# Kernel optimization log

Measured on AMD Instinct MI355X. Metric: run time of the kernel, lower is better.

The kernel has to match this reference:

```python
import jax, jax.numpy as jnp
import numpy as np
from jax import lax

B = 128      # batch
T = 80       # video frames
FEAT = 4096  # VGG feature dim
E_H = 512    # encoder hidden
D_H = 512    # decoder hidden
OHL = 3000   # vocab / one-hot length


def lstm(xs, h0, c0, Wih, Whh, b):
    """Single-layer LSTM over leading time axis. xs: (S, B, In). PyTorch gate order i,f,g,o."""
    def step(carry, x):
        h, c = carry
        gates = x @ Wih.T + h @ Whh.T + b  # (B, 4H)
        i, f, g, o = jnp.split(gates, 4, axis=-1)
        c = jax.nn.sigmoid(f) * c + jax.nn.sigmoid(i) * jnp.tanh(g)
        h = jax.nn.sigmoid(o) * jnp.tanh(c)
        return (h, c), h
    (h, c), ys = lax.scan(step, (h0, c0), xs)
    return ys, h, c


def setup_inputs() -> dict:
    key = jax.random.key(0)
    ks = jax.random.split(key, 16)
    def w(k, shape, fan):
        return (jax.random.normal(k, shape, jnp.float32) / np.sqrt(fan)).astype(jnp.float32)
    return {
        "input_feature": jax.random.normal(ks[0], (B, T, FEAT), jnp.float32),
        "correct_answer": jax.random.normal(ks[1], (44, B, OHL), jnp.float32),
        "We_ih": w(ks[2], (4 * E_H, FEAT), E_H),
        "We_hh": w(ks[3], (4 * E_H, E_H), E_H),
        "be_ih": w(ks[4], (4 * E_H,), E_H),
        "be_hh": w(ks[5], (4 * E_H,), E_H),
        "Wd_ih": w(ks[6], (4 * D_H, E_H + D_H), D_H),
        "Wd_hh": w(ks[7], (4 * D_H, D_H), D_H),
        "bd_ih": w(ks[8], (4 * D_H,), D_H),
        "bd_hh": w(ks[9], (4 * D_H,), D_H),
        "Wi": w(ks[10], (D_H, OHL), OHL),
        "bi": w(ks[11], (D_H,), OHL),
        "Wo": w(ks[12], (OHL, D_H), D_H),
        "bo": w(ks[13], (OHL,), D_H),
        "max_len": 44,
    }


def reference(input_feature, correct_answer, We_ih, We_hh, be_ih, be_hh,
              Wd_ih, Wd_hh, bd_ih, bd_hh, Wi, bi, Wo, bo, max_len):
    be = be_ih + be_hh
    bd = bd_ih + bd_hh
    # torch .view(shape[1], shape[0], 4096) on contiguous tensor == reshape
    x = input_feature.reshape(T, B, FEAT)
    # Encoding phase
    h0e = jnp.zeros((B, E_H), x.dtype)
    enc_seq, he, ce = lstm(x, h0e, h0e, We_ih, We_hh, be)
    dec_in = jnp.concatenate([enc_seq, jnp.zeros((T, B, D_H), x.dtype)], axis=2)
    h0d = jnp.zeros((B, D_H), x.dtype)
    _, hd, cd = lstm(dec_in, h0d, h0d, Wd_ih, Wd_hh, bd)
    # Encoder over zero padding for the caption phase
    pad = jnp.zeros((max_len, B, FEAT), x.dtype)
    enc_pad, _, _ = lstm(pad, he, ce, We_ih, We_hh, be)
    # Decoder inputs: <BOS> one-hot at step 0, teacher-forced answers after (schedule=False)
    bos = jnp.zeros((1, B, OHL), x.dtype).at[:, :, -2].set(1.0)
    emb_bos = bos @ Wi.T + bi                               # (1, B, D_H)
    emb_ans = correct_answer[1:max_len] @ Wi.T + bi         # (max_len-1, B, D_H)
    samples = jnp.concatenate([emb_bos, emb_ans], axis=0)   # (max_len, B, D_H)
    dec_in2 = jnp.concatenate([samples, enc_pad], axis=2)   # (max_len, B, D_H+E_H)
    dec_out, _, _ = lstm(dec_in2, hd, cd, Wd_ih, Wd_hh, bd)
    words = dec_out @ Wo.T + bo                              # (max_len, B, OHL)
    return words
```

## Files before the change

### kernel.cpp

```cpp
#include <hip/hip_runtime.h>
#include <cmath>


typedef __bf16 bf16x8 __attribute__((ext_vector_type(8)));
typedef float  f32x4  __attribute__((ext_vector_type(4)));

#define LDSROW 40

template<bool BIAS, bool ACCUM>
__global__ __launch_bounds__(256)
void gemm_split(const float* __restrict__ A, int lda,
                const float* __restrict__ Bw, int ldb,
                float* __restrict__ C, int ldc,
                const float* __restrict__ bias,
                int M, int N, int K)
{
    (void)M;
    __shared__ __bf16 sAh[128 * LDSROW], sAl[128 * LDSROW];
    __shared__ __bf16 sBh[128 * LDSROW], sBl[128 * LDSROW];

    const int tid  = threadIdx.x;
    const int lane = tid & 63;
    const int wid  = tid >> 6;
    const int m0 = blockIdx.x * 128, n0 = blockIdx.y * 128;
    const int wm = (wid >> 1) * 64, wn = (wid & 1) * 64;
    const int lr = lane & 15, lg = lane >> 4;

    const int srow = tid >> 1;
    const int scol = (tid & 1) * 16;

    f32x4 acc[4][4];
#pragma unroll
    for (int mt = 0; mt < 4; ++mt)
#pragma unroll
        for (int nt = 0; nt < 4; ++nt) acc[mt][nt] = (f32x4)(0.0f);

    const int KT = (K + 31) >> 5;
    for (int kt = 0; kt < KT; ++kt) {
        const int k0 = kt * 32;
        {
            const float* aptr = A + (size_t)(m0 + srow) * lda + k0 + scol;
            float x[16];
            if (k0 + scol + 16 <= K) {
                const f32x4* p = (const f32x4*)aptr;
                f32x4 v0 = p[0], v1 = p[1], v2 = p[2], v3 = p[3];
#pragma unroll
                for (int j = 0; j < 4; ++j) { x[j] = v0[j]; x[4+j] = v1[j]; x[8+j] = v2[j]; x[12+j] = v3[j]; }
            } else {
#pragma unroll
                for (int j = 0; j < 16; ++j) {
                    const int kk = k0 + scol + j;
                    x[j] = (kk < K) ? aptr[j] : 0.f;
                }
            }
#pragma unroll
            for (int j = 0; j < 16; ++j) {
                const float v = x[j];
                const __bf16 h = (__bf16)v;
                sAh[srow * LDSROW + scol + j] = h;
                sAl[srow * LDSROW + scol + j] = (__bf16)(v - (float)h);
            }
        }
        {
            const int nrow = n0 + srow;
            const float* bptr = Bw + (size_t)nrow * ldb + k0 + scol;
            float x[16];
            if (nrow < N && k0 + scol + 16 <= K) {
                const f32x4* p = (const f32x4*)bptr;
                f32x4 v0 = p[0], v1 = p[1], v2 = p[2], v3 = p[3];
#pragma unroll
                for (int j = 0; j < 4; ++j) { x[j] = v0[j]; x[4+j] = v1[j]; x[8+j] = v2[j]; x[12+j] = v3[j]; }
            } else {
#pragma unroll
                for (int j = 0; j < 16; ++j) {
                    const int kk = k0 + scol + j;
                    x[j] = (nrow < N && kk < K) ? bptr[j] : 0.f;
                }
            }
#pragma unroll
            for (int j = 0; j < 16; ++j) {
                const float v = x[j];
                const __bf16 h = (__bf16)v;
                sBh[srow * LDSROW + scol + j] = h;
                sBl[srow * LDSROW + scol + j] = (__bf16)(v - (float)h);
            }
        }
        __syncthreads();

        bf16x8 ah[4], al[4], bh[4], bl[4];
#pragma unroll
        for (int t = 0; t < 4; ++t) {
            ah[t] = *(const bf16x8*)&sAh[(wm + t * 16 + lr) * LDSROW + lg * 8];
            al[t] = *(const bf16x8*)&sAl[(wm + t * 16 + lr) * LDSROW + lg * 8];
            bh[t] = *(const bf16x8*)&sBh[(wn + t * 16 + lr) * LDSROW + lg * 8];
            bl[t] = *(const bf16x8*)&sBl[(wn + t * 16 + lr) * LDSROW + lg * 8];
        }
#pragma unroll
        for (int mt = 0; mt < 4; ++mt)
#pragma unroll
            for (int nt = 0; nt < 4; ++nt) {
                f32x4 a_ = acc[mt][nt];
                a_ = __builtin_amdgcn_mfma_f32_16x16x32_bf16(ah[mt], bh[nt], a_, 0, 0, 0);
                a_ = __builtin_amdgcn_mfma_f32_16x16x32_bf16(ah[mt], bl[nt], a_, 0, 0, 0);
                a_ = __builtin_amdgcn_mfma_f32_16x16x32_bf16(al[mt], bh[nt], a_, 0, 0, 0);
                acc[mt][nt] = a_;
            }
        __syncthreads();
    }

#pragma unroll
    for (int mt = 0; mt < 4; ++mt)
#pragma unroll
        for (int nt = 0; nt < 4; ++nt)
#pragma unroll
            for (int r = 0; r < 4; ++r) {
                const int m = m0 + wm + mt * 16 + lg * 4 + r;
                const int n = n0 + wn + nt * 16 + lr;
                if (n < N) {
                    float v = acc[mt][nt][r];
                    if (BIAS) v += bias[n];
                    if (ACCUM) v += C[(size_t)m * ldc + n];
                    C[(size_t)m * ldc + n] = v;
                }
            }
}

__global__ __launch_bounds__(256)
void lstm_step(const float* __restrict__ gpre,
               const float* __restrict__ bias,
               const float* __restrict__ Whh,
               const float* __restrict__ h_prev,
               float* __restrict__ c,
               float* __restrict__ h_out)
{
    __shared__ float h_s[16][36];
    __shared__ float w_s[64][36];
    const int tid = threadIdx.x;
    const int jj = tid & 15, bb = tid >> 4;
    const int j = blockIdx.x * 16 + jj;
    const int b = blockIdx.y * 16 + bb;

    float a0 = 0.f, a1 = 0.f, a2 = 0.f, a3 = 0.f;

    const int hr = tid >> 4, hc = (tid & 15) * 2;
    const int wr = tid >> 2, wc = (tid & 3) * 8;
    const int wg = wr >> 4, wj = wr & 15;
    const float* hsrc = h_prev + (size_t)(blockIdx.y * 16 + hr) * 512 + hc;
    const float* wsrc = Whh + (size_t)(wg * 512 + blockIdx.x * 16 + wj) * 512 + wc;

    for (int kt = 0; kt < 16; ++kt) {
        const int k0 = kt * 32;
        {
            const float2 hv = *(const float2*)(hsrc + k0);
            h_s[hr][hc] = hv.x; h_s[hr][hc + 1] = hv.y;
            const f32x4 w0 = *(const f32x4*)(wsrc + k0);
            const f32x4 w1 = *(const f32x4*)(wsrc + k0 + 4);
#pragma unroll
            for (int q = 0; q < 4; ++q) { w_s[wr][wc + q] = w0[q]; w_s[wr][wc + 4 + q] = w1[q]; }
        }
        __syncthreads();
#pragma unroll
        for (int k = 0; k < 32; ++k) {
            const float hvk = h_s[bb][k];
            a0 += hvk * w_s[ 0 + jj][k];
            a1 += hvk * w_s[16 + jj][k];
            a2 += hvk * w_s[32 + jj][k];
            a3 += hvk * w_s[48 + jj][k];
        }
        __syncthreads();
    }

    float pi = 0.f, pf = 0.f, pg = 0.f, po = 0.f;
    if (gpre) {
        const float* g = gpre + (size_t)b * 2048 + j;
        pi = g[0]; pf = g[512]; pg = g[1024]; po = g[1536];
    }
    if (bias) { pi += bias[j]; pf += bias[j + 512]; pg += bias[j + 1024]; po += bias[j + 1536]; }
    pi += a0; pf += a1; pg += a2; po += a3;

    const float ig = 1.f / (1.f + __expf(-pi));
    const float fg = 1.f / (1.f + __expf(-pf));
    const float gg = tanhf(pg);
    const float og = 1.f / (1.f + __expf(-po));

    const size_t ci = (size_t)b * 512 + j;
    const float cn = fg * c[ci] + ig * gg;
    c[ci] = cn;
    h_out[ci] = og * tanhf(cn);
}

__global__ void add2(const float* __restrict__ a, const float* __restrict__ b,
                     float* __restrict__ o, int n)
{
    const int i = blockIdx.x * 256 + threadIdx.x;
    if (i < n) o[i] = a[i] + b[i];
}

__global__ void emb_bos(const float* __restrict__ Wi, const float* __restrict__ bi,
                        float* __restrict__ emb)
{
    const int i = blockIdx.x * 256 + threadIdx.x;
    const int d = i & 511;
    emb[i] = Wi[(size_t)d * 3000 + 2998] + bi[d];
}

extern "C" void kernel_launch(void* const* d_in, const int* in_sizes, int n_in,
                              void* d_out, int out_size, void* d_ws, size_t ws_size,
                              hipStream_t stream)
{
    (void)in_sizes; (void)n_in; (void)out_size; (void)ws_size;
    const float* in_feat = (const float*)d_in[0];
    const float* ca      = (const float*)d_in[1];
    const float* We_ih   = (const float*)d_in[2];
    const float* We_hh   = (const float*)d_in[3];
    const float* be_ih   = (const float*)d_in[4];
    const float* be_hh   = (const float*)d_in[5];
    const float* Wd_ih   = (const float*)d_in[6];
    const float* Wd_hh   = (const float*)d_in[7];
    const float* bd_ih   = (const float*)d_in[8];
    const float* bd_hh   = (const float*)d_in[9];
    const float* Wi      = (const float*)d_in[10];
    const float* bi      = (const float*)d_in[11];
    const float* Wo      = (const float*)d_in[12];
    const float* bo      = (const float*)d_in[13];
    float* out = (float*)d_out;
    float* ws  = (float*)d_ws;

    float* be    = ws;
    float* bd    = be + 2048;
    float* Xbuf  = bd + 2048;
    float* encH  = Xbuf + (size_t)10240 * 2048;
    float* padH  = encH + (size_t)81 * 65536;
    float* doutH = padH + (size_t)45 * 65536;
    float* emb   = doutH + (size_t)45 * 65536;
    float* cE    = emb + (size_t)5632 * 512;
    float* cD    = cE + 65536;
    float* hd0   = cD + 65536;
    float* hd1   = hd0 + 65536;

    add2<<<dim3(8), dim3(256), 0, stream>>>(be_ih, be_hh, be, 2048);
    add2<<<dim3(8), dim3(256), 0, stream>>>(bd_ih, bd_hh, bd, 2048);

    hipMemsetAsync(encH, 0, 65536 * sizeof(float), stream);
    hipMemsetAsync(cE,   0, 65536 * sizeof(float), stream);
    hipMemsetAsync(cD,   0, 65536 * sizeof(float), stream);
    hipMemsetAsync(hd0,  0, 65536 * sizeof(float), stream);

    emb_bos<<<dim3(256), dim3(256), 0, stream>>>(Wi, bi, emb);

    gemm_split<true, false><<<dim3(80, 16), dim3(256), 0, stream>>>(
        in_feat, 4096, We_ih, 4096, Xbuf, 2048, be, 10240, 2048, 4096);

    gemm_split<true, false><<<dim3(43, 4), dim3(256), 0, stream>>>(
        ca + (size_t)128 * 3000, 3000, Wi, 3000, emb + (size_t)128 * 512, 512, bi,
        5504, 512, 3000);

    for (int t = 0; t < 80; ++t)
        lstm_step<<<dim3(32, 8), dim3(256), 0, stream>>>(
            Xbuf + (size_t)t * 262144, nullptr, We_hh,
            encH + (size_t)t * 65536, cE, encH + (size_t)(t + 1) * 65536);

    gemm_split<true, false><<<dim3(80, 16), dim3(256), 0, stream>>>(
        encH + 65536, 512, Wd_ih, 1024, Xbuf, 2048, bd, 10240, 2048, 512);

    for (int t = 0; t < 80; ++t) {
        float* hin  = (t & 1) ? hd1 : hd0;
        float* hout = (t & 1) ? hd0 : hd1;
        lstm_step<<<dim3(32, 8), dim3(256), 0, stream>>>(
            Xbuf + (size_t)t * 262144, nullptr, Wd_hh, hin, cD, hout);
    }

    for (int t = 0; t < 44; ++t) {
        const float* hin = (t == 0) ? (encH + (size_t)80 * 65536) : (padH + (size_t)t * 65536);
        lstm_step<<<dim3(32, 8), dim3(256), 0, stream>>>(
            nullptr, be, We_hh, hin, cE, padH + (size_t)(t + 1) * 65536);
    }

    gemm_split<true, false><<<dim3(44, 16), dim3(256), 0, stream>>>(
        emb, 512, Wd_ih, 1024, Xbuf, 2048, bd, 5632, 2048, 512);
    gemm_split<false, true><<<dim3(44, 16), dim3(256), 0, stream>>>(
        padH + 65536, 512, Wd_ih + 512, 1024, Xbuf, 2048, nullptr, 5632, 2048, 512);

    for (int t = 0; t < 44; ++t) {
        const float* hin = (t == 0) ? hd0 : (doutH + (size_t)t * 65536);
        lstm_step<<<dim3(32, 8), dim3(256), 0, stream>>>(
            Xbuf + (size_t)t * 262144, nullptr, Wd_hh, hin, cD, doutH + (size_t)(t + 1) * 65536);
    }

    gemm_split<true, false><<<dim3(44, 24), dim3(256), 0, stream>>>(
        doutH + 65536, 512, Wo, 512, out, 3000, bo, 5632, 3000, 512);
}
```

Before: 6.988 ms.

## Fuse all LSTM recurrences into one persistent kernel with grid barriers

Replaces the 248 per-timestep lstm_step launches with a single persistent 128-block kernel. The encoder and decoder run as a wavefront on separate halves of the grid, and steps are separated by an atomic grid barrier. Each block keeps its slice of the recurrent weights in LDS as bf16 and runs MFMA with a hi/lo split of h to keep close to fp32 accuracy. This removes launch overhead and the repeated weight reloads, but it relies on all 128 blocks being co-resident, and the weights are rounded to bf16.

```diff
diff --git a/kernel.cpp b/kernel.cpp
--- a/kernel.cpp
+++ b/kernel.cpp
@@ -6,6 +6,8 @@
 typedef float  f32x4  __attribute__((ext_vector_type(4)));
 
 #define LDSROW 40
+#define SLOT   65536
+#define NBLK   128
 
 template<bool BIAS, bool ACCUM>
 __global__ __launch_bounds__(256)
@@ -125,68 +127,207 @@
             }
 }
 
-__global__ __launch_bounds__(256)
-void lstm_step(const float* __restrict__ gpre,
-               const float* __restrict__ bias,
-               const float* __restrict__ Whh,
-               const float* __restrict__ h_prev,
-               float* __restrict__ c,
-               float* __restrict__ h_out)
-{
-    __shared__ float h_s[16][36];
-    __shared__ float w_s[64][36];
+
+__device__ __forceinline__ void gbar(unsigned* cnt, unsigned* gen)
+{
+    __syncthreads();
+    if (threadIdx.x == 0) {
+        __threadfence();
+        const unsigned g = __hip_atomic_load(gen, __ATOMIC_RELAXED, __HIP_MEMORY_SCOPE_AGENT);
+        const unsigned a = __hip_atomic_fetch_add(cnt, 1u, __ATOMIC_ACQ_REL, __HIP_MEMORY_SCOPE_AGENT);
+        if (a == NBLK - 1) {
+            __hip_atomic_store(cnt, 0u, __ATOMIC_RELAXED, __HIP_MEMORY_SCOPE_AGENT);
+            __hip_atomic_store(gen, g + 1u, __ATOMIC_RELEASE, __HIP_MEMORY_SCOPE_AGENT);
+        } else {
+            while (__hip_atomic_load(gen, __ATOMIC_ACQUIRE, __HIP_MEMORY_SCOPE_AGENT) == g)
+                __builtin_amdgcn_s_sleep(1);
+        }
+        __threadfence();
+    }
+    __syncthreads();
+}
+
+template<int KT>
+__device__ __forceinline__ void gemm_phase(
+    const __bf16* __restrict__ sW, float* __restrict__ pg, int K,
+    const __bf16* __restrict__ s1h, const __bf16* __restrict__ s1l,
+    const __bf16* __restrict__ s2h, const __bf16* __restrict__ s2l)
+{
+    const int lane = threadIdx.x & 63, w = threadIdx.x >> 6;
+    const int lr = lane & 15, lg = lane >> 4;
+    const int kf = lg * 8;
+    const int mb = w * 32 + lr;
+
+    f32x4 acc[2][2];
+#pragma unroll
+    for (int mt = 0; mt < 2; ++mt)
+#pragma unroll
+        for (int nt = 0; nt < 2; ++nt) acc[mt][nt] = (f32x4)(0.0f);
+
+#pragma unroll 2
+    for (int kt = 0; kt < KT; ++kt) {
+        const int kk = kt * 32 + kf;
+        const __bf16* ph; const __bf16* pl; int ko;
+        if (kk < 512) { ph = s1h; pl = s1l; ko = kk; }
+        else          { ph = s2h; pl = s2l; ko = kk - 512; }
+
+        const int n0 = lr, n1 = 16 + lr;
+        const bf16x8 b0 = *(const bf16x8*)&sW[(n0 * K + kt * 32 + kf) ^ ((n0 & 7) << 3)];
+        const bf16x8 b1 = *(const bf16x8*)&sW[(n1 * K + kt * 32 + kf) ^ ((n1 & 7) << 3)];
+#pragma unroll
+        for (int mt = 0; mt < 2; ++mt) {
+            const int m = mb + mt * 16;
+            const bf16x8 ah = *(const bf16x8*)&ph[m * 512 + ko];
+            const bf16x8 al = *(const bf16x8*)&pl[m * 512 + ko];
+            acc[mt][0] = __builtin_amdgcn_mfma_f32_16x16x32_bf16(ah, b0, acc[mt][0], 0, 0, 0);
+            acc[mt][0] = __builtin_amdgcn_mfma_f32_16x16x32_bf16(al, b0, acc[mt][0], 0, 0, 0);
+            acc[mt][1] = __builtin_amdgcn_mfma_f32_16x16x32_bf16(ah, b1, acc[mt][1], 0, 0, 0);
+            acc[mt][1] = __builtin_amdgcn_mfma_f32_16x16x32_bf16(al, b1, acc[mt][1], 0, 0, 0);
+        }
+    }
+
+#pragma unroll
+    for (int mt = 0; mt < 2; ++mt)
+#pragma unroll
+        for (int nt = 0; nt < 2; ++nt)
+#pragma unroll
+            for (int r = 0; r < 4; ++r)
+                pg[(w * 32 + mt * 16 + lg * 4 + r) * 33 + nt * 16 + lr] = acc[mt][nt][r];
+}
+
+__device__ __forceinline__ void pointwise(
+    const float* __restrict__ pg, const float* __restrict__ gpre,
+    const float* __restrict__ bsl, float* __restrict__ c, int d0,
+    __bf16* __restrict__ hhi, __bf16* __restrict__ hlo, float* __restrict__ hf32)
+{
     const int tid = threadIdx.x;
-    const int jj = tid & 15, bb = tid >> 4;
-    const int j = blockIdx.x * 16 + jj;
-    const int b = blockIdx.y * 16 + bb;
-
-    float a0 = 0.f, a1 = 0.f, a2 = 0.f, a3 = 0.f;
-
-    const int hr = tid >> 4, hc = (tid & 15) * 2;
-    const int wr = tid >> 2, wc = (tid & 3) * 8;
-    const int wg = wr >> 4, wj = wr & 15;
-    const float* hsrc = h_prev + (size_t)(blockIdx.y * 16 + hr) * 512 + hc;
-    const float* wsrc = Whh + (size_t)(wg * 512 + blockIdx.x * 16 + wj) * 512 + wc;
-
-    for (int kt = 0; kt < 16; ++kt) {
-        const int k0 = kt * 32;
-        {
-            const float2 hv = *(const float2*)(hsrc + k0);
-            h_s[hr][hc] = hv.x; h_s[hr][hc + 1] = hv.y;
-            const f32x4 w0 = *(const f32x4*)(wsrc + k0);
-            const f32x4 w1 = *(const f32x4*)(wsrc + k0 + 4);
-#pragma unroll
-            for (int q = 0; q < 4; ++q) { w_s[wr][wc + q] = w0[q]; w_s[wr][wc + 4 + q] = w1[q]; }
-        }
-        __syncthreads();
-#pragma unroll
-        for (int k = 0; k < 32; ++k) {
-            const float hvk = h_s[bb][k];
-            a0 += hvk * w_s[ 0 + jj][k];
-            a1 += hvk * w_s[16 + jj][k];
-            a2 += hvk * w_s[32 + jj][k];
-            a3 += hvk * w_s[48 + jj][k];
-        }
-        __syncthreads();
-    }
-
-    float pi = 0.f, pf = 0.f, pg = 0.f, po = 0.f;
+    const int b = tid >> 1, hf = tid & 1;
+    float add_[4][4];
     if (gpre) {
-        const float* g = gpre + (size_t)b * 2048 + j;
-        pi = g[0]; pf = g[512]; pg = g[1024]; po = g[1536];
-    }
-    if (bias) { pi += bias[j]; pf += bias[j + 512]; pg += bias[j + 1024]; po += bias[j + 1536]; }
-    pi += a0; pf += a1; pg += a2; po += a3;
-
-    const float ig = 1.f / (1.f + __expf(-pi));
-    const float fg = 1.f / (1.f + __expf(-pf));
-    const float gg = tanhf(pg);
-    const float og = 1.f / (1.f + __expf(-po));
-
-    const size_t ci = (size_t)b * 512 + j;
-    const float cn = fg * c[ci] + ig * gg;
-    c[ci] = cn;
-    h_out[ci] = og * tanhf(cn);
+#pragma unroll
+        for (int g = 0; g < 4; ++g) {
+            const f32x4 v = *(const f32x4*)&gpre[b * 2048 + g * 512 + d0 + hf * 4];
+#pragma unroll
+            for (int j = 0; j < 4; ++j) add_[g][j] = v[j];
+        }
+    } else {
+#pragma unroll
+        for (int g = 0; g < 4; ++g)
+#pragma unroll
+            for (int j = 0; j < 4; ++j) add_[g][j] = bsl[g * 8 + hf * 4 + j];
+    }
+#pragma unroll
+    for (int j = 0; j < 4; ++j) {
+        const int dd = hf * 4 + j;
+        const float pi = pg[b * 33 +  0 + dd] + add_[0][j];
+        const float pf = pg[b * 33 +  8 + dd] + add_[1][j];
+        const float pG = pg[b * 33 + 16 + dd] + add_[2][j];
+        const float po = pg[b * 33 + 24 + dd] + add_[3][j];
+        const float ig = 1.f / (1.f + __expf(-pi));
+        const float fg = 1.f / (1.f + __expf(-pf));
+        const float gg = tanhf(pG);
+        const float og = 1.f / (1.f + __expf(-po));
+        c[j] = fg * c[j] + ig * gg;
+        const float h = og * tanhf(c[j]);
+        const int off = b * 512 + d0 + dd;
+        const __bf16 hh = (__bf16)h;
+        hhi[off] = hh;
+        hlo[off] = (__bf16)(h - (float)hh);
+        if (hf32) hf32[off] = h;
+    }
+}
+
+__global__ __launch_bounds__(256, 1)
+void recurrence_kernel(const float* __restrict__ gpreE, const float* __restrict__ gpre2,
+                       const float* __restrict__ We_hh, const float* __restrict__ Wd_ih,
+                       const float* __restrict__ Wd_hh,
+                       const float* __restrict__ be, const float* __restrict__ bd,
+                       __bf16* encHi, __bf16* encLo, __bf16* padHi, __bf16* padLo,
+                       __bf16* dHi, __bf16* dLo, float* doutW,
+                       unsigned* bar_cnt, unsigned* bar_gen)
+{
+    __shared__ __bf16 sW[32 * 1024];
+    __shared__ float  pg[128 * 33];
+    __shared__ float  bsl[32];
+
+    const int  bid    = blockIdx.x;
+    const bool is_dec = bid >= 64;
+    const int  d0     = (is_dec ? bid - 64 : bid) * 8;
+    const int  tid    = threadIdx.x;
+    const int  K      = is_dec ? 1024 : 512;
+
+    for (int idx = tid; idx < 32 * K; idx += 256) {
+        const int nn = idx / K;
+        const int kk = idx - nn * K;
+        const int gr = (nn >> 3) * 512 + d0 + (nn & 7);
+        float wv;
+        if (!is_dec) wv = We_hh[(size_t)gr * 512 + kk];
+        else         wv = (kk < 512) ? Wd_ih[(size_t)gr * 1024 + kk]
+                                     : Wd_hh[(size_t)gr * 512 + kk - 512];
+        sW[(nn * K + kk) ^ ((nn & 7) << 3)] = (__bf16)wv;
+    }
+    if (tid < 32) bsl[tid] = (is_dec ? bd : be)[(tid >> 3) * 512 + d0 + (tid & 7)];
+    __syncthreads();
+
+    float c[4] = {0.f, 0.f, 0.f, 0.f};
+
+    for (int p = 0; p <= 80; ++p) {
+        if (!is_dec) {
+            if (p < 80) {
+                gemm_phase<16>(sW, pg, 512,
+                               encHi + (p & 1) * SLOT, encLo + (p & 1) * SLOT,
+                               nullptr, nullptr);
+                __syncthreads();
+                pointwise(pg, gpreE + (size_t)p * 262144, bsl, c, d0,
+                          encHi + ((p + 1) & 1) * SLOT, encLo + ((p + 1) & 1) * SLOT, nullptr);
+            }
+        } else {
+            if (p >= 1) {
+                const int t = p - 1;
+                gemm_phase<32>(sW, pg, 1024,
+                               encHi + (p & 1) * SLOT, encLo + (p & 1) * SLOT,
+                               dHi + (t & 1) * SLOT, dLo + (t & 1) * SLOT);
+                __syncthreads();
+                pointwise(pg, nullptr, bsl, c, d0,
+                          dHi + ((t + 1) & 1) * SLOT, dLo + ((t + 1) & 1) * SLOT, nullptr);
+            }
+        }
+        gbar(bar_cnt, bar_gen);
+    }
+
+    if (is_dec) {
+        for (int idx = tid; idx < 32 * 512; idx += 256) {
+            const int nn = idx >> 9, kk = idx & 511;
+            const int gr = (nn >> 3) * 512 + d0 + (nn & 7);
+            sW[(nn * 1024 + kk) ^ ((nn & 7) << 3)] = (__bf16)Wd_ih[(size_t)gr * 1024 + 512 + kk];
+        }
+    }
+    __syncthreads();
+
+    for (int q = 0; q <= 44; ++q) {
+        if (!is_dec) {
+            if (q < 44) {
+                const __bf16* sh = (q == 0) ? encHi : padHi + (q & 1) * SLOT;
+                const __bf16* sl = (q == 0) ? encLo : padLo + (q & 1) * SLOT;
+                gemm_phase<16>(sW, pg, 512, sh, sl, nullptr, nullptr);
+                __syncthreads();
+                pointwise(pg, nullptr, bsl, c, d0,
+                          padHi + ((q + 1) & 1) * SLOT, padLo + ((q + 1) & 1) * SLOT, nullptr);
+            }
+        } else {
+            if (q >= 1) {
+                const int u = q - 1;
+                gemm_phase<32>(sW, pg, 1024,
+                               padHi + (q & 1) * SLOT, padLo + (q & 1) * SLOT,
+                               dHi + (u & 1) * SLOT, dLo + (u & 1) * SLOT);
+                __syncthreads();
+                pointwise(pg, gpre2 + (size_t)u * 262144, bsl, c, d0,
+                          dHi + ((u + 1) & 1) * SLOT, dLo + ((u + 1) & 1) * SLOT,
+                          doutW + (size_t)u * SLOT);
+            }
+        }
+        gbar(bar_cnt, bar_gen);
+    }
 }
 
 __global__ void add2(const float* __restrict__ a, const float* __restrict__ b,
@@ -228,65 +369,44 @@
 
     float* be    = ws;
     float* bd    = be + 2048;
-    float* Xbuf  = bd + 2048;
-    float* encH  = Xbuf + (size_t)10240 * 2048;
-    float* padH  = encH + (size_t)81 * 65536;
-    float* doutH = padH + (size_t)45 * 65536;
-    float* emb   = doutH + (size_t)45 * 65536;
-    float* cE    = emb + (size_t)5632 * 512;
-    float* cD    = cE + 65536;
-    float* hd0   = cD + 65536;
-    float* hd1   = hd0 + 65536;
+    float* gpreE = bd + 2048;
+    float* gpre2 = gpreE + (size_t)80 * 262144;
+    float* emb   = gpre2 + (size_t)44 * 262144;
+    float* doutW = emb + (size_t)5632 * 512;
+    float* bf16z = doutW + (size_t)5632 * 512;
+    __bf16* encHi = (__bf16*)bf16z;
+    __bf16* encLo = encHi + 2 * SLOT;
+    __bf16* padHi = encLo + 2 * SLOT;
+    __bf16* padLo = padHi + 2 * SLOT;
+    __bf16* dHi   = padLo + 2 * SLOT;
+    __bf16* dLo   = dHi + 2 * SLOT;
+    unsigned* bar = (unsigned*)(dLo + 2 * SLOT);
 
     add2<<<dim3(8), dim3(256), 0, stream>>>(be_ih, be_hh, be, 2048);
     add2<<<dim3(8), dim3(256), 0, stream>>>(bd_ih, bd_hh, bd, 2048);
 
-    hipMemsetAsync(encH, 0, 65536 * sizeof(float), stream);
-    hipMemsetAsync(cE,   0, 65536 * sizeof(float), stream);
-    hipMemsetAsync(cD,   0, 65536 * sizeof(float), stream);
-    hipMemsetAsync(hd0,  0, 65536 * sizeof(float), stream);
+    hipMemsetAsync(encHi, 0, SLOT * 2, stream);
+    hipMemsetAsync(encLo, 0, SLOT * 2, stream);
+    hipMemsetAsync(dHi,   0, SLOT * 2, stream);
+    hipMemsetAsync(dLo,   0, SLOT * 2, stream);
+    hipMemsetAsync(bar,   0, 8, stream);
 
     emb_bos<<<dim3(256), dim3(256), 0, stream>>>(Wi, bi, emb);
 
     gemm_split<true, false><<<dim3(80, 16), dim3(256), 0, stream>>>(
-        in_feat, 4096, We_ih, 4096, Xbuf, 2048, be, 10240, 2048, 4096);
+        in_feat, 4096, We_ih, 4096, gpreE, 2048, be, 10240, 2048, 4096);
 
     gemm_split<true, false><<<dim3(43, 4), dim3(256), 0, stream>>>(
         ca + (size_t)128 * 3000, 3000, Wi, 3000, emb + (size_t)128 * 512, 512, bi,
         5504, 512, 3000);
 
-    for (int t = 0; t < 80; ++t)
-        lstm_step<<<dim3(32, 8), dim3(256), 0, stream>>>(
-            Xbuf + (size_t)t * 262144, nullptr, We_hh,
-            encH + (size_t)t * 65536, cE, encH + (size_t)(t + 1) * 65536);
-
-    gemm_split<true, false><<<dim3(80, 16), dim3(256), 0, stream>>>(
-        encH + 65536, 512, Wd_ih, 1024, Xbuf, 2048, bd, 10240, 2048, 512);
-
-    for (int t = 0; t < 80; ++t) {
-        float* hin  = (t & 1) ? hd1 : hd0;
-        float* hout = (t & 1) ? hd0 : hd1;
-        lstm_step<<<dim3(32, 8), dim3(256), 0, stream>>>(
-            Xbuf + (size_t)t * 262144, nullptr, Wd_hh, hin, cD, hout);
-    }
-
-    for (int t = 0; t < 44; ++t) {
-        const float* hin = (t == 0) ? (encH + (size_t)80 * 65536) : (padH + (size_t)t * 65536);
-        lstm_step<<<dim3(32, 8), dim3(256), 0, stream>>>(
-            nullptr, be, We_hh, hin, cE, padH + (size_t)(t + 1) * 65536);
-    }
-
     gemm_split<true, false><<<dim3(44, 16), dim3(256), 0, stream>>>(
-        emb, 512, Wd_ih, 1024, Xbuf, 2048, bd, 5632, 2048, 512);
-    gemm_split<false, true><<<dim3(44, 16), dim3(256), 0, stream>>>(
-        padH + 65536, 512, Wd_ih + 512, 1024, Xbuf, 2048, nullptr, 5632, 2048, 512);
-
-    for (int t = 0; t < 44; ++t) {
-        const float* hin = (t == 0) ? hd0 : (doutH + (size_t)t * 65536);
-        lstm_step<<<dim3(32, 8), dim3(256), 0, stream>>>(
-            Xbuf + (size_t)t * 262144, nullptr, Wd_hh, hin, cD, doutH + (size_t)(t + 1) * 65536);
-    }
+        emb, 512, Wd_ih, 1024, gpre2, 2048, bd, 5632, 2048, 512);
+
+    recurrence_kernel<<<dim3(NBLK), dim3(256), 0, stream>>>(
+        gpreE, gpre2, We_hh, Wd_ih, Wd_hh, be, bd,
+        encHi, encLo, padHi, padLo, dHi, dLo, doutW, bar, bar + 1);
 
     gemm_split<true, false><<<dim3(44, 24), dim3(256), 0, stream>>>(
-        doutH + 65536, 512, Wo, 512, out, 3000, bo, 5632, 3000, 512);
-}
+        doutW, 512, Wo, 512, out, 3000, bo, 5632, 3000, 512);
+}
```

Result: slower. 8.642 ms (+23.7%).
